# Kernel tuning notes

Hardware: AMD Instinct MI355X
Metric: run time of the kernel (lower is better)

The kernel has to match this reference:

```python
import jax, jax.numpy as jnp
import numpy as np

ALPHA = 0.2      # LeakyReLU negative slope
NEG_INF = -9e15  # mask fill value from the original


def setup_inputs() -> dict:
    key = jax.random.key(0)
    ks = jax.random.split(key, 6)
    B, N, C, E = 2, 1024, 32, 32  # in_channels == embed_dim (required by bias add)
    x = jax.random.normal(ks[0], (B, N, C), dtype=jnp.float32)
    adj = jax.random.randint(ks[1], (B, N, N), 0, 2, dtype=jnp.int32)
    W1 = jax.random.normal(ks[2], (C, E), dtype=jnp.float32) * 0.1
    W2 = jax.random.normal(ks[3], (2 * C, E), dtype=jnp.float32) * 0.1
    a = jax.random.normal(ks[4], (E, 1), dtype=jnp.float32) * 0.1
    bias = jax.random.normal(ks[5], (E,), dtype=jnp.float32) * 0.1
    return {"x": x, "adj": adj, "W1": W1, "W2": W2, "a": a, "bias": bias}


def reference(x, adj, W1, W2, a, bias):
    B, N, C = x.shape
    # dead code in the original (hidden is never used) -- W1 gets zero grad
    _hidden = jnp.matmul(x, W1)
    # faithful replication of the original's (buggy but deterministic) layout:
    # cat along the flattened pair axis, then view as (B, N, N, 2C)
    rep_chunks = jnp.repeat(x, N, axis=1)       # (B, N*N, C): row k -> x[k//N]
    rep_alt = jnp.tile(x, (1, N, 1))            # (B, N*N, C): row k -> x[k%N]
    all_comb = jnp.concatenate([rep_chunks, rep_alt], axis=1).reshape(B, N, N, 2 * C)
    wx = jnp.einsum('bijc,ce->bije', all_comb, W2)          # (B,N,N,E)
    attn = jax.nn.leaky_relu(wx, negative_slope=ALPHA)
    scores = jnp.einsum('bije,eo->bijo', attn, a)[..., 0]   # (B,N,N)
    scores = jnp.where(adj > 0, scores, NEG_INF)
    attention = jax.nn.softmax(scores, axis=-1)             # dropout: identity (eval)
    out = jnp.matmul(attention, x) + bias                   # (B,N,C), C == E
    return jnp.tanh(out)
```

## Files before the change

### kernel.cpp

```cpp
#include <hip/hip_runtime.h>
#include <math.h>

#define ALPHA 0.2f

constexpr int N = 1024;
constexpr int C = 32;

__global__ __launch_bounds__(256) void uvexp_kernel(
    const float* __restrict__ x, const float* __restrict__ W2,
    const float* __restrict__ a, float* __restrict__ eu, float* __restrict__ ev)
{
    __shared__ float sW2[64 * 32];
    __shared__ float sa[32];
    const int tid = threadIdx.x;
    for (int idx = tid; idx < 64 * 32; idx += 256) sW2[idx] = W2[idx];
    if (tid < 32) sa[tid] = a[tid];
    __syncthreads();

    const int gout = (blockIdx.x * 256 + tid) >> 5;
    const int e = tid & 31;
    const int isV = gout >> 11;
    const int idx = gout & 2047;
    const int b = idx >> 10;
    const int n = idx & 1023;
    const float* xb = x + b * (N * C);

    float acc = 0.f;
    if (!isV) {
        const float* xr = xb + n * 32;
        #pragma unroll
        for (int c = 0; c < 32; ++c) {
            const float xv = xr[c];
            acc = fmaf(xv, sW2[c * 32 + e], acc);
            acc = fmaf(xv, sW2[(c + 32) * 32 + e], acc);
        }
    } else {
        const float* x0 = xb + ((2 * n) & 1023) * 32;
        const float* x1 = xb + ((2 * n + 1) & 1023) * 32;
        #pragma unroll
        for (int c = 0; c < 32; ++c) {
            acc = fmaf(x0[c], sW2[c * 32 + e], acc);
            acc = fmaf(x1[c], sW2[(c + 32) * 32 + e], acc);
        }
    }
    float t = (acc > 0.f ? acc : ALPHA * acc) * sa[e];
    #pragma unroll
    for (int m = 16; m >= 1; m >>= 1) t += __shfl_xor(t, m);
    if (e == 0) (isV ? ev : eu)[idx] = expf(t);
}

__global__ __launch_bounds__(256) void attn_kernel4(
    const float* __restrict__ x, const int* __restrict__ adj,
    const float* __restrict__ eu, const float* __restrict__ ev,
    const float* __restrict__ bias, float* __restrict__ out)
{
    __shared__ float swT[1024 * 4];
    __shared__ float partF[4 * 4 * 32];
    __shared__ float wsred[4 * 4];

    const int tid = threadIdx.x;
    const int row0 = blockIdx.x * 4;
    const int b = row0 >> 10;
    const int i0 = row0 & 1023;
    const int wave = tid >> 6;
    const int lane = tid & 63;

    float w[4][4];
    if (i0 < 512) {
        float su[4][2];
        #pragma unroll
        for (int r = 0; r < 4; ++r) {
            su[r][0] = eu[(b << 10) + 2 * (i0 + r)];
            su[r][1] = eu[(b << 10) + 2 * (i0 + r) + 1];
        }
        #pragma unroll
        for (int m = 0; m < 4; ++m) {
            const int half = m >> 1;
            #pragma unroll
            for (int r = 0; r < 4; ++r) {
                const int aij = adj[(size_t)(row0 + r) * 1024 + tid + 256 * m];
                w[m][r] = aij > 0 ? su[r][half] : 0.f;
            }
        }
    } else {
        #pragma unroll
        for (int m = 0; m < 4; ++m) {
            const float evj = ev[(b << 10) + tid + 256 * m];
            #pragma unroll
            for (int r = 0; r < 4; ++r) {
                const int aij = adj[(size_t)(row0 + r) * 1024 + tid + 256 * m];
                w[m][r] = aij > 0 ? evj : 0.f;
            }
        }
    }
    float ws[4];
    #pragma unroll
    for (int r = 0; r < 4; ++r)
        ws[r] = (w[0][r] + w[1][r]) + (w[2][r] + w[3][r]);
    #pragma unroll
    for (int m = 0; m < 4; ++m)
        ((float4*)swT)[tid + 256 * m] = make_float4(w[m][0], w[m][1], w[m][2], w[m][3]);
    #pragma unroll
    for (int s = 32; s >= 1; s >>= 1) {
        ws[0] += __shfl_xor(ws[0], s);
        ws[1] += __shfl_xor(ws[1], s);
        ws[2] += __shfl_xor(ws[2], s);
        ws[3] += __shfl_xor(ws[3], s);
    }
    if (lane == 0) {
        #pragma unroll
        for (int r = 0; r < 4; ++r) wsred[wave * 4 + r] = ws[r];
    }
    __syncthreads();

    const float4* x4 = (const float4*)(x + b * (N * C));
    const int c4 = tid & 7;
    const int jg = tid >> 3;
    float4 a0 = make_float4(0.f, 0.f, 0.f, 0.f);
    float4 a1 = a0, a2 = a0, a3 = a0;
    #pragma unroll 8
    for (int q = 0; q < 32; ++q) {
        const int j = jg * 32 + ((q + jg) & 31);
        const float4 wv = ((const float4*)swT)[j];
        const float4 xv = x4[j * 8 + c4];
        a0.x = fmaf(wv.x, xv.x, a0.x); a0.y = fmaf(wv.x, xv.y, a0.y);
        a0.z = fmaf(wv.x, xv.z, a0.z); a0.w = fmaf(wv.x, xv.w, a0.w);
        a1.x = fmaf(wv.y, xv.x, a1.x); a1.y = fmaf(wv.y, xv.y, a1.y);
        a1.z = fmaf(wv.y, xv.z, a1.z); a1.w = fmaf(wv.y, xv.w, a1.w);
        a2.x = fmaf(wv.z, xv.x, a2.x); a2.y = fmaf(wv.z, xv.y, a2.y);
        a2.z = fmaf(wv.z, xv.z, a2.z); a2.w = fmaf(wv.z, xv.w, a2.w);
        a3.x = fmaf(wv.w, xv.x, a3.x); a3.y = fmaf(wv.w, xv.y, a3.y);
        a3.z = fmaf(wv.w, xv.z, a3.z); a3.w = fmaf(wv.w, xv.w, a3.w);
    }
    #pragma unroll
    for (int s = 8; s <= 32; s <<= 1) {
        a0.x += __shfl_xor(a0.x, s); a0.y += __shfl_xor(a0.y, s);
        a0.z += __shfl_xor(a0.z, s); a0.w += __shfl_xor(a0.w, s);
        a1.x += __shfl_xor(a1.x, s); a1.y += __shfl_xor(a1.y, s);
        a1.z += __shfl_xor(a1.z, s); a1.w += __shfl_xor(a1.w, s);
        a2.x += __shfl_xor(a2.x, s); a2.y += __shfl_xor(a2.y, s);
        a2.z += __shfl_xor(a2.z, s); a2.w += __shfl_xor(a2.w, s);
        a3.x += __shfl_xor(a3.x, s); a3.y += __shfl_xor(a3.y, s);
        a3.z += __shfl_xor(a3.z, s); a3.w += __shfl_xor(a3.w, s);
    }
    if (lane < 8) {
        ((float4*)partF)[(wave * 4 + 0) * 8 + c4] = a0;
        ((float4*)partF)[(wave * 4 + 1) * 8 + c4] = a1;
        ((float4*)partF)[(wave * 4 + 2) * 8 + c4] = a2;
        ((float4*)partF)[(wave * 4 + 3) * 8 + c4] = a3;
    }
    __syncthreads();

    if (tid < 128) {
        const int r = tid >> 5, c = tid & 31;
        float o = (partF[(0 * 4 + r) * 32 + c] + partF[(1 * 4 + r) * 32 + c]) +
                  (partF[(2 * 4 + r) * 32 + c] + partF[(3 * 4 + r) * 32 + c]);
        float dn = (wsred[0 * 4 + r] + wsred[1 * 4 + r]) +
                   (wsred[2 * 4 + r] + wsred[3 * 4 + r]);
        if (dn == 0.f) {
            o = 0.f;
            for (int j = 0; j < 1024; ++j) o += x[b * (N * C) + j * 32 + c];
            dn = 1024.f;
        }
        out[(size_t)(row0 + r) * 32 + c] = tanhf(fmaf(o, 1.0f / dn, bias[c]));
    }
}

extern "C" void kernel_launch(void* const* d_in, const int* in_sizes, int n_in,
                              void* d_out, int out_size, void* d_ws, size_t ws_size,
                              hipStream_t stream) {
    const float* x    = (const float*)d_in[0];
    const int*   adj  = (const int*)d_in[1];
    const float* W2   = (const float*)d_in[3];
    const float* a    = (const float*)d_in[4];
    const float* bias = (const float*)d_in[5];
    float* out = (float*)d_out;

    float* eu = (float*)d_ws;
    float* ev = eu + 2 * 1024;

    uvexp_kernel<<<512, 256, 0, stream>>>(x, W2, a, eu, ev);
    attn_kernel4<<<512, 256, 0, stream>>>(x, adj, eu, ev, bias, out);
}
```

Baseline: 78.28 us.

## Fuse score precompute and attention into one cooperative kernel with grid sync

Merges the exp-score precompute kernel and the attention aggregation kernel into a single cooperative launch separated by a grid-wide barrier. The adjacency loads are issued before the barrier so their memory latency overlaps the score phase and the sync. This removes one kernel launch and the inter-kernel gap. In exchange it pays for a grid sync and cooperative-launch overhead, and W2 is now read from global memory rather than staged in shared memory.

```diff
diff --git a/kernel.cpp b/kernel.cpp
--- a/kernel.cpp
+++ b/kernel.cpp
@@ -1,69 +1,74 @@
 #include <hip/hip_runtime.h>
+#include <hip/hip_cooperative_groups.h>
 #include <math.h>
+
+namespace cg = cooperative_groups;
 
 #define ALPHA 0.2f
 
 constexpr int N = 1024;
 constexpr int C = 32;
 
-__global__ __launch_bounds__(256) void uvexp_kernel(
-    const float* __restrict__ x, const float* __restrict__ W2,
-    const float* __restrict__ a, float* __restrict__ eu, float* __restrict__ ev)
-{
-    __shared__ float sW2[64 * 32];
-    __shared__ float sa[32];
-    const int tid = threadIdx.x;
-    for (int idx = tid; idx < 64 * 32; idx += 256) sW2[idx] = W2[idx];
-    if (tid < 32) sa[tid] = a[tid];
-    __syncthreads();
-
-    const int gout = (blockIdx.x * 256 + tid) >> 5;
-    const int e = tid & 31;
-    const int isV = gout >> 11;
-    const int idx = gout & 2047;
-    const int b = idx >> 10;
-    const int n = idx & 1023;
-    const float* xb = x + b * (N * C);
-
-    float acc = 0.f;
-    if (!isV) {
-        const float* xr = xb + n * 32;
-        #pragma unroll
-        for (int c = 0; c < 32; ++c) {
-            const float xv = xr[c];
-            acc = fmaf(xv, sW2[c * 32 + e], acc);
-            acc = fmaf(xv, sW2[(c + 32) * 32 + e], acc);
-        }
-    } else {
-        const float* x0 = xb + ((2 * n) & 1023) * 32;
-        const float* x1 = xb + ((2 * n + 1) & 1023) * 32;
-        #pragma unroll
-        for (int c = 0; c < 32; ++c) {
-            acc = fmaf(x0[c], sW2[c * 32 + e], acc);
-            acc = fmaf(x1[c], sW2[(c + 32) * 32 + e], acc);
-        }
-    }
-    float t = (acc > 0.f ? acc : ALPHA * acc) * sa[e];
-    #pragma unroll
-    for (int m = 16; m >= 1; m >>= 1) t += __shfl_xor(t, m);
-    if (e == 0) (isV ? ev : eu)[idx] = expf(t);
-}
-
-__global__ __launch_bounds__(256) void attn_kernel4(
+__global__ __launch_bounds__(256) void fused_gat_kernel(
     const float* __restrict__ x, const int* __restrict__ adj,
-    const float* __restrict__ eu, const float* __restrict__ ev,
-    const float* __restrict__ bias, float* __restrict__ out)
+    const float* __restrict__ W2, const float* __restrict__ a,
+    const float* __restrict__ bias, float* __restrict__ eu,
+    float* __restrict__ ev, float* __restrict__ out)
 {
     __shared__ float swT[1024 * 4];
     __shared__ float partF[4 * 4 * 32];
     __shared__ float wsred[4 * 4];
 
     const int tid = threadIdx.x;
+
+    {
+        const int gout = blockIdx.x * 8 + (tid >> 5);
+        const int e = tid & 31;
+        const int isV = gout >> 11;
+        const int idx = gout & 2047;
+        const int b = idx >> 10;
+        const int n = idx & 1023;
+        const float* xb = x + b * (N * C);
+
+        float acc = 0.f;
+        if (!isV) {
+            const float* xr = xb + n * 32;
+            #pragma unroll
+            for (int c = 0; c < 32; ++c) {
+                const float xv = xr[c];
+                acc = fmaf(xv, W2[c * 32 + e], acc);
+                acc = fmaf(xv, W2[(c + 32) * 32 + e], acc);
+            }
+        } else {
+            const float* x0 = xb + ((2 * n) & 1023) * 32;
+            const float* x1 = xb + ((2 * n + 1) & 1023) * 32;
+            #pragma unroll
+            for (int c = 0; c < 32; ++c) {
+                acc = fmaf(x0[c], W2[c * 32 + e], acc);
+                acc = fmaf(x1[c], W2[(c + 32) * 32 + e], acc);
+            }
+        }
+        float t = (acc > 0.f ? acc : ALPHA * acc) * a[e];
+        #pragma unroll
+        for (int m = 16; m >= 1; m >>= 1) t += __shfl_xor(t, m);
+        if (e == 0) (isV ? ev : eu)[idx] = expf(t);
+    }
+
     const int row0 = blockIdx.x * 4;
     const int b = row0 >> 10;
     const int i0 = row0 & 1023;
     const int wave = tid >> 6;
     const int lane = tid & 63;
+
+    int aij[4][4];
+    #pragma unroll
+    for (int m = 0; m < 4; ++m) {
+        #pragma unroll
+        for (int r = 0; r < 4; ++r)
+            aij[m][r] = adj[(size_t)(row0 + r) * 1024 + tid + 256 * m];
+    }
+
+    cg::this_grid().sync();
 
     float w[4][4];
     if (i0 < 512) {
@@ -77,20 +82,16 @@
         for (int m = 0; m < 4; ++m) {
             const int half = m >> 1;
             #pragma unroll
-            for (int r = 0; r < 4; ++r) {
-                const int aij = adj[(size_t)(row0 + r) * 1024 + tid + 256 * m];
-                w[m][r] = aij > 0 ? su[r][half] : 0.f;
-            }
+            for (int r = 0; r < 4; ++r)
+                w[m][r] = aij[m][r] > 0 ? su[r][half] : 0.f;
         }
     } else {
         #pragma unroll
         for (int m = 0; m < 4; ++m) {
             const float evj = ev[(b << 10) + tid + 256 * m];
             #pragma unroll
-            for (int r = 0; r < 4; ++r) {
-                const int aij = adj[(size_t)(row0 + r) * 1024 + tid + 256 * m];
-                w[m][r] = aij > 0 ? evj : 0.f;
-            }
+            for (int r = 0; r < 4; ++r)
+                w[m][r] = aij[m][r] > 0 ? evj : 0.f;
         }
     }
     float ws[4];
@@ -179,6 +180,8 @@
     float* eu = (float*)d_ws;
     float* ev = eu + 2 * 1024;
 
-    uvexp_kernel<<<512, 256, 0, stream>>>(x, W2, a, eu, ev);
-    attn_kernel4<<<512, 256, 0, stream>>>(x, adj, eu, ev, bias, out);
+    void* args[] = {(void*)&x, (void*)&adj, (void*)&W2, (void*)&a,
+                    (void*)&bias, (void*)&eu, (void*)&ev, (void*)&out};
+    hipLaunchCooperativeKernel((const void*)fused_gat_kernel,
+                               dim3(512), dim3(256), args, 0, stream);
 }
```

New measurement: 128.3 us. 63.9% more time.

## Fuse score precompute into attention kernel and process eight rows per block

Applied to the files above, without the earlier changes.

Merges the separate exp-score kernel into the attention kernel, so each block recomputes the exponentiated u/v scores it needs into shared memory instead of reading them from a workspace buffer. Blocks grow to 512 threads covering 8 rows, halving the grid, and the adjacency loads are issued before the score computation so they can overlap with it. This removes one kernel launch and the global round trip for the intermediates. The cost is redundant per-block score computation, especially the 32-wide per-thread accumulation for the v scores, plus higher register pressure.

```diff
diff --git a/kernel.cpp b/kernel.cpp
--- a/kernel.cpp
+++ b/kernel.cpp
@@ -5,161 +5,172 @@
 
 constexpr int N = 1024;
 constexpr int C = 32;
+constexpr int R = 8;
+constexpr int T = 512;
 
-__global__ __launch_bounds__(256) void uvexp_kernel(
-    const float* __restrict__ x, const float* __restrict__ W2,
-    const float* __restrict__ a, float* __restrict__ eu, float* __restrict__ ev)
+__global__ __launch_bounds__(T) void gat_fused(
+    const float* __restrict__ x, const int* __restrict__ adj,
+    const float* __restrict__ W2, const float* __restrict__ a,
+    const float* __restrict__ bias, float* __restrict__ out)
 {
     __shared__ float sW2[64 * 32];
     __shared__ float sa[32];
-    const int tid = threadIdx.x;
-    for (int idx = tid; idx < 64 * 32; idx += 256) sW2[idx] = W2[idx];
-    if (tid < 32) sa[tid] = a[tid];
-    __syncthreads();
-
-    const int gout = (blockIdx.x * 256 + tid) >> 5;
-    const int e = tid & 31;
-    const int isV = gout >> 11;
-    const int idx = gout & 2047;
-    const int b = idx >> 10;
-    const int n = idx & 1023;
-    const float* xb = x + b * (N * C);
-
-    float acc = 0.f;
-    if (!isV) {
-        const float* xr = xb + n * 32;
-        #pragma unroll
-        for (int c = 0; c < 32; ++c) {
-            const float xv = xr[c];
-            acc = fmaf(xv, sW2[c * 32 + e], acc);
-            acc = fmaf(xv, sW2[(c + 32) * 32 + e], acc);
-        }
-    } else {
-        const float* x0 = xb + ((2 * n) & 1023) * 32;
-        const float* x1 = xb + ((2 * n + 1) & 1023) * 32;
-        #pragma unroll
-        for (int c = 0; c < 32; ++c) {
-            acc = fmaf(x0[c], sW2[c * 32 + e], acc);
-            acc = fmaf(x1[c], sW2[(c + 32) * 32 + e], acc);
-        }
-    }
-    float t = (acc > 0.f ? acc : ALPHA * acc) * sa[e];
-    #pragma unroll
-    for (int m = 16; m >= 1; m >>= 1) t += __shfl_xor(t, m);
-    if (e == 0) (isV ? ev : eu)[idx] = expf(t);
-}
-
-__global__ __launch_bounds__(256) void attn_kernel4(
-    const float* __restrict__ x, const int* __restrict__ adj,
-    const float* __restrict__ eu, const float* __restrict__ ev,
-    const float* __restrict__ bias, float* __restrict__ out)
-{
-    __shared__ float swT[1024 * 4];
-    __shared__ float partF[4 * 4 * 32];
-    __shared__ float wsred[4 * 4];
+    __shared__ float sev[512];
+    __shared__ float swT[1024 * R];
+    __shared__ float partF[8 * R * 32];
+    __shared__ float wsred[8 * R];
 
     const int tid = threadIdx.x;
-    const int row0 = blockIdx.x * 4;
+    const int row0 = blockIdx.x * R;
     const int b = row0 >> 10;
     const int i0 = row0 & 1023;
     const int wave = tid >> 6;
     const int lane = tid & 63;
+    const float* xb = x + b * (N * C);
 
-    float w[4][4];
+    int aij[2][R];
+    #pragma unroll
+    for (int h = 0; h < 2; ++h)
+        #pragma unroll
+        for (int r = 0; r < R; ++r)
+            aij[h][r] = adj[(size_t)(row0 + r) * 1024 + tid + 512 * h];
+
+    #pragma unroll
+    for (int k = 0; k < 4; ++k) sW2[tid + 512 * k] = W2[tid + 512 * k];
+    if (tid < 32) sa[tid] = a[tid];
+    __syncthreads();
+
     if (i0 < 512) {
-        float su[4][2];
+        const int k = tid >> 5;
+        const int e = tid & 31;
+        const float* xr = xb + (2 * i0 + k) * 32;
+        float acc = 0.f;
         #pragma unroll
-        for (int r = 0; r < 4; ++r) {
-            su[r][0] = eu[(b << 10) + 2 * (i0 + r)];
-            su[r][1] = eu[(b << 10) + 2 * (i0 + r) + 1];
-        }
+        for (int c2 = 0; c2 < 32; ++c2)
+            acc = fmaf(xr[c2], sW2[c2 * 32 + e] + sW2[(c2 + 32) * 32 + e], acc);
+        float t = (acc > 0.f ? acc : ALPHA * acc) * sa[e];
         #pragma unroll
-        for (int m = 0; m < 4; ++m) {
-            const int half = m >> 1;
+        for (int m = 16; m >= 1; m >>= 1) t += __shfl_xor(t, m);
+        if (e == 0) sev[k] = expf(t);
+    } else {
+        float z[32];
+        #pragma unroll
+        for (int e = 0; e < 32; ++e) z[e] = 0.f;
+        const float4* x04 = (const float4*)(xb + 2 * tid * 32);
+        #pragma unroll
+        for (int c4 = 0; c4 < 16; ++c4) {
+            const float4 f = x04[c4];
+            const int cbase = c4 * 4;
             #pragma unroll
-            for (int r = 0; r < 4; ++r) {
-                const int aij = adj[(size_t)(row0 + r) * 1024 + tid + 256 * m];
-                w[m][r] = aij > 0 ? su[r][half] : 0.f;
+            for (int cc = 0; cc < 4; ++cc) {
+                const float xv = (&f.x)[cc];
+                const float* wrow = &sW2[(cbase + cc) * 32];
+                #pragma unroll
+                for (int e = 0; e < 32; ++e) z[e] = fmaf(xv, wrow[e], z[e]);
             }
         }
+        float sc = 0.f;
+        #pragma unroll
+        for (int e = 0; e < 32; ++e) {
+            const float tv = z[e] > 0.f ? z[e] : ALPHA * z[e];
+            sc = fmaf(tv, sa[e], sc);
+        }
+        sev[tid] = expf(sc);
+    }
+    __syncthreads();
+
+    float w[2][R];
+    if (i0 < 512) {
+        #pragma unroll
+        for (int h = 0; h < 2; ++h)
+            #pragma unroll
+            for (int r = 0; r < R; ++r)
+                w[h][r] = aij[h][r] > 0 ? sev[2 * r + h] : 0.f;
     } else {
+        const float evj = sev[tid];
         #pragma unroll
-        for (int m = 0; m < 4; ++m) {
-            const float evj = ev[(b << 10) + tid + 256 * m];
+        for (int h = 0; h < 2; ++h)
             #pragma unroll
-            for (int r = 0; r < 4; ++r) {
-                const int aij = adj[(size_t)(row0 + r) * 1024 + tid + 256 * m];
-                w[m][r] = aij > 0 ? evj : 0.f;
-            }
-        }
+            for (int r = 0; r < R; ++r)
+                w[h][r] = aij[h][r] > 0 ? evj : 0.f;
     }
-    float ws[4];
     #pragma unroll
-    for (int r = 0; r < 4; ++r)
-        ws[r] = (w[0][r] + w[1][r]) + (w[2][r] + w[3][r]);
+    for (int h = 0; h < 2; ++h) {
+        const int j = tid + 512 * h;
+        ((float4*)swT)[j * 2 + 0] = make_float4(w[h][0], w[h][1], w[h][2], w[h][3]);
+        ((float4*)swT)[j * 2 + 1] = make_float4(w[h][4], w[h][5], w[h][6], w[h][7]);
+    }
+    float ws[R];
     #pragma unroll
-    for (int m = 0; m < 4; ++m)
-        ((float4*)swT)[tid + 256 * m] = make_float4(w[m][0], w[m][1], w[m][2], w[m][3]);
+    for (int r = 0; r < R; ++r) ws[r] = w[0][r] + w[1][r];
     #pragma unroll
     for (int s = 32; s >= 1; s >>= 1) {
-        ws[0] += __shfl_xor(ws[0], s);
-        ws[1] += __shfl_xor(ws[1], s);
-        ws[2] += __shfl_xor(ws[2], s);
-        ws[3] += __shfl_xor(ws[3], s);
+        #pragma unroll
+        for (int r = 0; r < R; ++r) ws[r] += __shfl_xor(ws[r], s);
     }
     if (lane == 0) {
         #pragma unroll
-        for (int r = 0; r < 4; ++r) wsred[wave * 4 + r] = ws[r];
+        for (int r = 0; r < R; ++r) wsred[wave * R + r] = ws[r];
     }
     __syncthreads();
 
-    const float4* x4 = (const float4*)(x + b * (N * C));
+    const float4* x4 = (const float4*)xb;
     const int c4 = tid & 7;
     const int jg = tid >> 3;
-    float4 a0 = make_float4(0.f, 0.f, 0.f, 0.f);
-    float4 a1 = a0, a2 = a0, a3 = a0;
-    #pragma unroll 8
-    for (int q = 0; q < 32; ++q) {
-        const int j = jg * 32 + ((q + jg) & 31);
-        const float4 wv = ((const float4*)swT)[j];
+    float4 acc[R];
+    #pragma unroll
+    for (int r = 0; r < R; ++r) acc[r] = make_float4(0.f, 0.f, 0.f, 0.f);
+    #pragma unroll 4
+    for (int q = 0; q < 16; ++q) {
+        const int j = jg * 16 + q;
+        const float4 w0 = ((const float4*)swT)[j * 2 + 0];
+        const float4 w1 = ((const float4*)swT)[j * 2 + 1];
         const float4 xv = x4[j * 8 + c4];
-        a0.x = fmaf(wv.x, xv.x, a0.x); a0.y = fmaf(wv.x, xv.y, a0.y);
-        a0.z = fmaf(wv.x, xv.z, a0.z); a0.w = fmaf(wv.x, xv.w, a0.w);
-        a1.x = fmaf(wv.y, xv.x, a1.x); a1.y = fmaf(wv.y, xv.y, a1.y);
-        a1.z = fmaf(wv.y, xv.z, a1.z); a1.w = fmaf(wv.y, xv.w, a1.w);
-        a2.x = fmaf(wv.z, xv.x, a2.x); a2.y = fmaf(wv.z, xv.y, a2.y);
-        a2.z = fmaf(wv.z, xv.z, a2.z); a2.w = fmaf(wv.z, xv.w, a2.w);
-        a3.x = fmaf(wv.w, xv.x, a3.x); a3.y = fmaf(wv.w, xv.y, a3.y);
-        a3.z = fmaf(wv.w, xv.z, a3.z); a3.w = fmaf(wv.w, xv.w, a3.w);
+        acc[0].x = fmaf(w0.x, xv.x, acc[0].x); acc[0].y = fmaf(w0.x, xv.y, acc[0].y);
+        acc[0].z = fmaf(w0.x, xv.z, acc[0].z); acc[0].w = fmaf(w0.x, xv.w, acc[0].w);
+        acc[1].x = fmaf(w0.y, xv.x, acc[1].x); acc[1].y = fmaf(w0.y, xv.y, acc[1].y);
+        acc[1].z = fmaf(w0.y, xv.z, acc[1].z); acc[1].w = fmaf(w0.y, xv.w, acc[1].w);
+        acc[2].x = fmaf(w0.z, xv.x, acc[2].x); acc[2].y = fmaf(w0.z, xv.y, acc[2].y);
+        acc[2].z = fmaf(w0.z, xv.z, acc[2].z); acc[2].w = fmaf(w0.z, xv.w, acc[2].w);
+        acc[3].x = fmaf(w0.w, xv.x, acc[3].x); acc[3].y = fmaf(w0.w, xv.y, acc[3].y);
+        acc[3].z = fmaf(w0.w, xv.z, acc[3].z); acc[3].w = fmaf(w0.w, xv.w, acc[3].w);
+        acc[4].x = fmaf(w1.x, xv.x, acc[4].x); acc[4].y = fmaf(w1.x, xv.y, acc[4].y);
+        acc[4].z = fmaf(w1.x, xv.z, acc[4].z); acc[4].w = fmaf(w1.x, xv.w, acc[4].w);
+        acc[5].x = fmaf(w1.y, xv.x, acc[5].x); acc[5].y = fmaf(w1.y, xv.y, acc[5].y);
+        acc[5].z = fmaf(w1.y, xv.z, acc[5].z); acc[5].w = fmaf(w1.y, xv.w, acc[5].w);
+        acc[6].x = fmaf(w1.z, xv.x, acc[6].x); acc[6].y = fmaf(w1.z, xv.y, acc[6].y);
+        acc[6].z = fmaf(w1.z, xv.z, acc[6].z); acc[6].w = fmaf(w1.z, xv.w, acc[6].w);
+        acc[7].x = fmaf(w1.w, xv.x, acc[7].x); acc[7].y = fmaf(w1.w, xv.y, acc[7].y);
+        acc[7].z = fmaf(w1.w, xv.z, acc[7].z); acc[7].w = fmaf(w1.w, xv.w, acc[7].w);
     }
     #pragma unroll
     for (int s = 8; s <= 32; s <<= 1) {
-        a0.x += __shfl_xor(a0.x, s); a0.y += __shfl_xor(a0.y, s);
-        a0.z += __shfl_xor(a0.z, s); a0.w += __shfl_xor(a0.w, s);
-        a1.x += __shfl_xor(a1.x, s); a1.y += __shfl_xor(a1.y, s);
-        a1.z += __shfl_xor(a1.z, s); a1.w += __shfl_xor(a1.w, s);
-        a2.x += __shfl_xor(a2.x, s); a2.y += __shfl_xor(a2.y, s);
-        a2.z += __shfl_xor(a2.z, s); a2.w += __shfl_xor(a2.w, s);
-        a3.x += __shfl_xor(a3.x, s); a3.y += __shfl_xor(a3.y, s);
-        a3.z += __shfl_xor(a3.z, s); a3.w += __shfl_xor(a3.w, s);
+        #pragma unroll
+        for (int r = 0; r < R; ++r) {
+            acc[r].x += __shfl_xor(acc[r].x, s);
+            acc[r].y += __shfl_xor(acc[r].y, s);
+            acc[r].z += __shfl_xor(acc[r].z, s);
+            acc[r].w += __shfl_xor(acc[r].w, s);
+        }
     }
     if (lane < 8) {
-        ((float4*)partF)[(wave * 4 + 0) * 8 + c4] = a0;
-        ((float4*)partF)[(wave * 4 + 1) * 8 + c4] = a1;
-        ((float4*)partF)[(wave * 4 + 2) * 8 + c4] = a2;
-        ((float4*)partF)[(wave * 4 + 3) * 8 + c4] = a3;
+        #pragma unroll
+        for (int r = 0; r < R; ++r)
+            ((float4*)partF)[(wave * R + r) * 8 + c4] = acc[r];
     }
     __syncthreads();
 
-    if (tid < 128) {
+    if (tid < 256) {
         const int r = tid >> 5, c = tid & 31;
-        float o = (partF[(0 * 4 + r) * 32 + c] + partF[(1 * 4 + r) * 32 + c]) +
-                  (partF[(2 * 4 + r) * 32 + c] + partF[(3 * 4 + r) * 32 + c]);
-        float dn = (wsred[0 * 4 + r] + wsred[1 * 4 + r]) +
-                   (wsred[2 * 4 + r] + wsred[3 * 4 + r]);
+        float o = 0.f, dn = 0.f;
+        #pragma unroll
+        for (int wv = 0; wv < 8; ++wv) {
+            o  += partF[(wv * R + r) * 32 + c];
+            dn += wsred[wv * R + r];
+        }
         if (dn == 0.f) {
             o = 0.f;
-            for (int j = 0; j < 1024; ++j) o += x[b * (N * C) + j * 32 + c];
+            for (int j = 0; j < 1024; ++j) o += xb[j * 32 + c];
             dn = 1024.f;
         }
         out[(size_t)(row0 + r) * 32 + c] = tanhf(fmaf(o, 1.0f / dn, bias[c]));
@@ -176,9 +187,5 @@
     const float* bias = (const float*)d_in[5];
     float* out = (float*)d_out;
 
-    float* eu = (float*)d_ws;
-    float* ev = eu + 2 * 1024;
-
-    uvexp_kernel<<<512, 256, 0, stream>>>(x, W2, a, eu, ev);
-    attn_kernel4<<<512, 256, 0, stream>>>(x, adj, eu, ev, bias, out);
+    gat_fused<<<256, T, 0, stream>>>(x, adj, W2, a, bias, out);
 }
```

Measured after the change: 85.12 us. 1.09x slower.
